# Kernel tuning notes

Measured on AMD Instinct MI355X. Metric: run time of the kernel, lower is better.

## Reference

```python
import jax, jax.numpy as jnp
import numpy as np
import math

D_MODEL = 256
N_HEADS = 8
HEAD_DIM = D_MODEL // N_HEADS  # 32
N_LEVELS = 4
N_POINTS = 4
SHAPES = [(112, 112), (56, 56), (28, 28), (14, 14)]
LEN_IN = sum(h * w for h, w in SHAPES)  # 16660
BATCH = 1
LEN_Q = LEN_IN


def _grid_init_bias():
    # Faithful to MSDeformAttn._reset_parameters: directional grid init for sampling_offsets bias.
    thetas = np.arange(N_HEADS, dtype=np.float32) * (2.0 * math.pi / N_HEADS)
    grid = np.stack([np.cos(thetas), np.sin(thetas)], -1)
    grid = grid / np.abs(grid).max(-1, keepdims=True)
    grid = np.tile(grid[:, None, None, :], (1, N_LEVELS, N_POINTS, 1)).copy()
    for i in range(N_POINTS):
        grid[:, :, i, :] *= i + 1
    return jnp.asarray(grid.reshape(-1), dtype=jnp.float32)


def setup_inputs() -> dict:
    key = jax.random.key(0)
    ks = jax.random.split(key, 10)
    s = 1.0 / math.sqrt(D_MODEL)
    return {
        "query": jax.random.normal(ks[0], (BATCH, LEN_Q, D_MODEL), jnp.float32),
        "reference_points": jax.random.uniform(ks[1], (BATCH, LEN_Q, N_LEVELS, 2), jnp.float32),
        "input_flatten": jax.random.normal(ks[2], (BATCH, LEN_IN, D_MODEL), jnp.float32),
        "spatial_shapes": jnp.asarray(SHAPES, dtype=jnp.int32),
        "level_start_index": jnp.asarray(np.cumsum([0] + [h * w for h, w in SHAPES])[:-1], dtype=jnp.int32),
        "W_q": jax.random.normal(ks[3], (D_MODEL, D_MODEL), jnp.float32) * s,
        "b_q": jnp.zeros((D_MODEL,), jnp.float32),
        "W_k": jax.random.normal(ks[4], (D_MODEL, D_MODEL), jnp.float32) * s,
        "b_k": jnp.zeros((D_MODEL,), jnp.float32),
        "W_v": jax.random.normal(ks[5], (D_MODEL, D_MODEL), jnp.float32) * s,
        "b_v": jnp.zeros((D_MODEL,), jnp.float32),
        "W_o": jax.random.normal(ks[6], (D_MODEL, D_MODEL), jnp.float32) * s,
        "b_o": jnp.zeros((D_MODEL,), jnp.float32),
        "W_off": jax.random.normal(ks[7], (D_MODEL, N_HEADS * N_LEVELS * N_POINTS * 2), jnp.float32) * 0.01,
        "b_off": _grid_init_bias(),
    }


def _bilinear_sample(img, grid, H, W):
    # img: (B, H*W, D) flattened feature map; grid: (B, Q, P, 2) in [-1, 1] (x, y order).
    # Matches F.grid_sample(mode='bilinear', padding_mode='zeros', align_corners=False).
    B, Q, P, _ = grid.shape
    x = ((grid[..., 0] + 1.0) * W - 1.0) * 0.5
    y = ((grid[..., 1] + 1.0) * H - 1.0) * 0.5
    x0 = jnp.floor(x)
    y0 = jnp.floor(y)
    lx = x - x0
    ly = y - y0
    x0i = x0.astype(jnp.int32)
    y0i = y0.astype(jnp.int32)

    def gather(yi, xi, w):
        valid = (xi >= 0) & (xi < W) & (yi >= 0) & (yi < H)
        idx = jnp.clip(yi, 0, H - 1) * W + jnp.clip(xi, 0, W - 1)
        v = jnp.take_along_axis(img, idx.reshape(B, Q * P, 1), axis=1)
        return v.reshape(B, Q, P, -1) * (w * valid)[..., None]

    return (gather(y0i, x0i, (1.0 - ly) * (1.0 - lx))
            + gather(y0i, x0i + 1, (1.0 - ly) * lx)
            + gather(y0i + 1, x0i, ly * (1.0 - lx))
            + gather(y0i + 1, x0i + 1, ly * lx))


def reference(query, reference_points, input_flatten, spatial_shapes, level_start_index,
              W_q, b_q, W_k, b_k, W_v, b_v, W_o, b_o, W_off, b_off):
    N, Lq, C = query.shape
    M, D, L, P = N_HEADS, HEAD_DIM, N_LEVELS, N_POINTS

    q = query @ W_q + b_q                                   # (N, Lq, C)
    value = (input_flatten @ W_v + b_v).reshape(N, -1, M, D)
    key_h = (input_flatten @ W_k + b_k).reshape(N, -1, M, D)

    offsets = (q @ W_off + b_off).reshape(N, Lq, M, L, P, 2)
    # offset_normalizer = (W_l, H_l) per level
    norm = jnp.stack([spatial_shapes[:, 1], spatial_shapes[:, 0]], -1).astype(q.dtype)
    loc = reference_points[:, :, None, :, None, :] + offsets / norm[None, None, None, :, None, :]
    grids = 2.0 * loc - 1.0                                  # (N, Lq, M, L, P, 2)

    samp_v, samp_k = [], []
    start = 0
    for lid, (H, W) in enumerate(SHAPES):
        end = start + H * W
        v_l = value[:, start:end].transpose(0, 2, 1, 3).reshape(N * M, H * W, D)
        k_l = key_h[:, start:end].transpose(0, 2, 1, 3).reshape(N * M, H * W, D)
        g_l = grids[:, :, :, lid].transpose(0, 2, 1, 3, 4).reshape(N * M, Lq, P, 2)
        samp_v.append(_bilinear_sample(v_l, g_l, H, W))      # (N*M, Lq, P, D)
        samp_k.append(_bilinear_sample(k_l, g_l, H, W))
        start = end

    v_s = jnp.stack(samp_v, axis=2).reshape(N, M, Lq, L, P, D)
    k_s = jnp.stack(samp_k, axis=2).reshape(N, M, Lq, L, P, D)

    qh = q.reshape(N, Lq, M, D)
    logits = jnp.einsum('nqmd,nmqlpd->nmqlp', qh, k_s) / math.sqrt(D)
    attn = jax.nn.softmax(logits.reshape(N, M, Lq, L * P), axis=-1).reshape(N, M, Lq, L, P)

    out = jnp.einsum('nmqlp,nmqlpd->nqmd', attn, v_s).reshape(N, Lq, C)
    return out @ W_o + b_o
```

## Files before the change

kernel.cpp:

```cpp
#include <hip/hip_runtime.h>
#include <hip/hip_bf16.h>
#include <math.h>

#define LEN_IN   16660
#define D_MODEL  256
#define N_HEADS  8
#define HEAD_DIM 32
#define N_LEVELS 4
#define N_POINTS 4

typedef __attribute__((ext_vector_type(8))) short short8v;
typedef __attribute__((ext_vector_type(4))) float f32x4;
typedef _Float16 f16x2 __attribute__((ext_vector_type(2)));
typedef _Float16 f16x8 __attribute__((ext_vector_type(8)));

__device__ __forceinline__ unsigned f2h16(float f) {
  _Float16 h = (_Float16)f;
  union { unsigned short u; _Float16 h; } c;
  c.h = h;
  return (unsigned)c.u;
}
__device__ __forceinline__ f16x2 u2h(unsigned u) {
  union { unsigned u; f16x2 h; } c;
  c.u = u;
  return c.h;
}

__global__ __launch_bounds__(256) void prep_B(
    const float* __restrict__ Wq, const float* __restrict__ Wk,
    const float* __restrict__ Wv, const float* __restrict__ Woff,
    const float* __restrict__ Wo,
    unsigned short* __restrict__ Btq, unsigned short* __restrict__ Btk,
    unsigned short* __restrict__ Btv, unsigned short* __restrict__ Btoff,
    unsigned short* __restrict__ Bto) {
  __shared__ float tile[64][65];
  int b = blockIdx.x;
  int mat = b >> 4, t = b & 15;
  int ti = t >> 2, tj = t & 3;
  const float* W = (mat == 0) ? Wq : (mat == 1) ? Wk : (mat == 2) ? Wv
                 : (mat == 3) ? Woff : Wo;
  unsigned short* Bt = (mat == 0) ? Btq : (mat == 1) ? Btk : (mat == 2) ? Btv
                     : (mat == 3) ? Btoff : Bto;
  int tid = threadIdx.x;
  #pragma unroll
  for (int i = 0; i < 16; i++) {
    int idx = tid + i * 256;
    int kr = idx >> 6, nc = idx & 63;
    tile[kr][nc] = W[(size_t)(ti * 64 + kr) * 256 + tj * 64 + nc];
  }
  __syncthreads();
  #pragma unroll
  for (int i = 0; i < 16; i++) {
    int idx = tid + i * 256;
    int nr = idx >> 6, kc = idx & 63;
    Bt[(size_t)(tj * 64 + nr) * 256 + ti * 64 + kc] =
        (unsigned short)f2h16(tile[kc][nr]);
  }
}

__global__ __launch_bounds__(256) void gemm_f16(
    const float* __restrict__ A,
    const unsigned short* __restrict__ Bt,
    const float* __restrict__ bias, float* __restrict__ C, int M) {
  const int P = 40;
  __shared__ short As[64 * P], Bs[64 * P];
  int tid = threadIdx.x;
  int m0 = blockIdx.x * 64, n0 = blockIdx.y * 64;
  int w = tid >> 6, l = tid & 63;
  int r = l & 15, g = l >> 4;
  int mi = (w >> 1) * 32, ni = (w & 1) * 32;
  int sm = tid >> 2, sp = tid & 3;

  f32x4 acc[2][2];
  #pragma unroll
  for (int a = 0; a < 2; a++)
    #pragma unroll
    for (int b = 0; b < 2; b++) acc[a][b] = (f32x4){0.f, 0.f, 0.f, 0.f};

  for (int k0 = 0; k0 < 256; k0 += 32) {
    int gm = m0 + sm;
    float f[8];
    if (gm < M) {
      const float* src = A + (size_t)gm * 256 + k0 + sp * 8;
      float4 u0 = *(const float4*)src;
      float4 u1 = *(const float4*)(src + 4);
      f[0] = u0.x; f[1] = u0.y; f[2] = u0.z; f[3] = u0.w;
      f[4] = u1.x; f[5] = u1.y; f[6] = u1.z; f[7] = u1.w;
    } else {
      #pragma unroll
      for (int j = 0; j < 8; j++) f[j] = 0.f;
    }
    f16x8 hv;
    #pragma unroll
    for (int j = 0; j < 8; j++) hv[j] = (_Float16)f[j];
    *(f16x8*)&As[sm * P + sp * 8] = hv;
    *(short8v*)&Bs[sm * P + sp * 8] =
        *(const short8v*)&Bt[(size_t)(n0 + sm) * 256 + k0 + sp * 8];
    __syncthreads();

    f16x8 af[2], bf[2];
    #pragma unroll
    for (int a = 0; a < 2; a++)
      af[a] = *(f16x8*)&As[(mi + a * 16 + r) * P + g * 8];
    #pragma unroll
    for (int b = 0; b < 2; b++)
      bf[b] = *(f16x8*)&Bs[(ni + b * 16 + r) * P + g * 8];
    #pragma unroll
    for (int a = 0; a < 2; a++)
      #pragma unroll
      for (int b = 0; b < 2; b++)
        acc[a][b] = __builtin_amdgcn_mfma_f32_16x16x32_f16(af[a], bf[b], acc[a][b], 0, 0, 0);
    __syncthreads();
  }

  #pragma unroll
  for (int a = 0; a < 2; a++)
    #pragma unroll
    for (int b = 0; b < 2; b++) {
      int col = n0 + ni + b * 16 + r;
      float bc = bias[col];
      #pragma unroll
      for (int i = 0; i < 4; i++) {
        int row = m0 + mi + a * 16 + g * 4 + i;
        if (row < M) C[(size_t)row * 256 + col] = acc[a][b][i] + bc;
      }
    }
}

__global__ __launch_bounds__(256) void gemm_kv_f16(
    const float* __restrict__ A,
    const unsigned short* __restrict__ Btk,
    const unsigned short* __restrict__ Btv,
    const float* __restrict__ bk, const float* __restrict__ bv,
    unsigned* __restrict__ kvout, int M) {
  const int P = 40;
  __shared__ short As[64 * P], Bks[64 * P], Bvs[64 * P];
  int tid = threadIdx.x;
  int m0 = blockIdx.x * 64, n0 = blockIdx.y * 64;
  int w = tid >> 6, l = tid & 63;
  int r = l & 15, g = l >> 4;
  int mi = (w >> 1) * 32, ni = (w & 1) * 32;
  int sm = tid >> 2, sp = tid & 3;

  f32x4 acck[2][2], accv[2][2];
  #pragma unroll
  for (int a = 0; a < 2; a++)
    #pragma unroll
    for (int b = 0; b < 2; b++) {
      acck[a][b] = (f32x4){0.f, 0.f, 0.f, 0.f};
      accv[a][b] = (f32x4){0.f, 0.f, 0.f, 0.f};
    }

  for (int k0 = 0; k0 < 256; k0 += 32) {
    int gm = m0 + sm;
    float f[8];
    if (gm < M) {
      const float* src = A + (size_t)gm * 256 + k0 + sp * 8;
      float4 u0 = *(const float4*)src;
      float4 u1 = *(const float4*)(src + 4);
      f[0] = u0.x; f[1] = u0.y; f[2] = u0.z; f[3] = u0.w;
      f[4] = u1.x; f[5] = u1.y; f[6] = u1.z; f[7] = u1.w;
    } else {
      #pragma unroll
      for (int j = 0; j < 8; j++) f[j] = 0.f;
    }
    f16x8 hv;
    #pragma unroll
    for (int j = 0; j < 8; j++) hv[j] = (_Float16)f[j];
    *(f16x8*)&As[sm * P + sp * 8] = hv;
    *(short8v*)&Bks[sm * P + sp * 8] =
        *(const short8v*)&Btk[(size_t)(n0 + sm) * 256 + k0 + sp * 8];
    *(short8v*)&Bvs[sm * P + sp * 8] =
        *(const short8v*)&Btv[(size_t)(n0 + sm) * 256 + k0 + sp * 8];
    __syncthreads();

    f16x8 af[2], fbk[2], fbv[2];
    #pragma unroll
    for (int a = 0; a < 2; a++)
      af[a] = *(f16x8*)&As[(mi + a * 16 + r) * P + g * 8];
    #pragma unroll
    for (int b = 0; b < 2; b++) {
      fbk[b] = *(f16x8*)&Bks[(ni + b * 16 + r) * P + g * 8];
      fbv[b] = *(f16x8*)&Bvs[(ni + b * 16 + r) * P + g * 8];
    }
    #pragma unroll
    for (int a = 0; a < 2; a++)
      #pragma unroll
      for (int b = 0; b < 2; b++) {
        acck[a][b] = __builtin_amdgcn_mfma_f32_16x16x32_f16(af[a], fbk[b], acck[a][b], 0, 0, 0);
        accv[a][b] = __builtin_amdgcn_mfma_f32_16x16x32_f16(af[a], fbv[b], accv[a][b], 0, 0, 0);
      }
    __syncthreads();
  }

  #pragma unroll
  for (int a = 0; a < 2; a++)
    #pragma unroll
    for (int b = 0; b < 2; b++) {
      int col = n0 + ni + b * 16 + r;
      float bkc = bk[col], bvc = bv[col];
      #pragma unroll
      for (int i = 0; i < 4; i++) {
        int row = m0 + mi + a * 16 + g * 4 + i;
        if (row < M) {
          unsigned kh = f2h16(acck[a][b][i] + bkc);
          unsigned vh = f2h16(accv[a][b][i] + bvc);
          kvout[(size_t)row * 256 + col] = kh | (vh << 16);
        }
      }
    }
}

__global__ __launch_bounds__(256) void sample_attn(
    const float* __restrict__ qp,
    const float* __restrict__ offs,
    const float* __restrict__ rp,
    const unsigned* __restrict__ kv,
    float* __restrict__ attn_out) {
  __shared__ float lbuf[4][16];
  __shared__ float ebuf[4][16];
  __shared__ float vbuf[4][16][36];

  int tid = threadIdx.x;
  int wslot = tid >> 6;
  int lane = tid & 63;
  int wid = blockIdx.x * 4 + wslot;
  int q = wid >> 3;
  int h = wid & 7;

  int pt = lane >> 2;
  int c8 = (lane & 3) * 8;
  int l5 = lane & 31;

  float offv = offs[(size_t)q * D_MODEL + h * 32 + l5];
  float rpv = (l5 < 8) ? rp[(size_t)q * 8 + l5] : 0.f;

  int l = pt >> 2, pp = pt & 3;
  int W = 112 >> l;
  int start = (int)((50176u - (50176u >> (2 * l))) / 3u);

  float off_x = __shfl(offv, l * 8 + pp * 2 + 0, 64);
  float off_y = __shfl(offv, l * 8 + pp * 2 + 1, 64);
  float rp_x = __shfl(rpv, l * 2 + 0, 64);
  float rp_y = __shfl(rpv, l * 2 + 1, 64);

  float x = rp_x * (float)W + off_x - 0.5f;
  float y = rp_y * (float)W + off_y - 0.5f;
  float x0f = floorf(x), y0f = floorf(y);
  float lx = x - x0f, ly = y - y0f;
  int x0 = (int)x0f, y0 = (int)y0f;
  float wx0 = 1.f - lx, wy0 = 1.f - ly;
  float tw[4] = {wy0 * wx0, wy0 * lx, ly * wx0, ly * lx};

  int hoff = h * 32 + c8;

  f16x2 acc[8];
  #pragma unroll
  for (int j = 0; j < 8; j++) acc[j] = (f16x2){(_Float16)0.f, (_Float16)0.f};

  #pragma unroll
  for (int tap = 0; tap < 4; tap++) {
    int yy = y0 + (tap >> 1), xx = x0 + (tap & 1);
    bool valid = ((unsigned)xx < (unsigned)W) & ((unsigned)yy < (unsigned)W);
    float wgt = valid ? tw[tap] : 0.f;
    int pix = valid ? (start + yy * W + xx) : start;
    const unsigned* p = kv + (size_t)pix * D_MODEL + hoff;
    uint4 u0 = *(const uint4*)p;
    uint4 u1 = *(const uint4*)(p + 4);
    _Float16 wh = (_Float16)wgt;
    f16x2 w2 = {wh, wh};
    acc[0] += w2 * u2h(u0.x);
    acc[1] += w2 * u2h(u0.y);
    acc[2] += w2 * u2h(u0.z);
    acc[3] += w2 * u2h(u0.w);
    acc[4] += w2 * u2h(u1.x);
    acc[5] += w2 * u2h(u1.y);
    acc[6] += w2 * u2h(u1.z);
    acc[7] += w2 * u2h(u1.w);
  }

  const float* qsrc = qp + (size_t)q * D_MODEL + hoff;
  float4 qa = *(const float4*)qsrc;
  float4 qb = *(const float4*)(qsrc + 4);
  float dot = qa.x * (float)acc[0][0] + qa.y * (float)acc[1][0]
            + qa.z * (float)acc[2][0] + qa.w * (float)acc[3][0]
            + qb.x * (float)acc[4][0] + qb.y * (float)acc[5][0]
            + qb.z * (float)acc[6][0] + qb.w * (float)acc[7][0];
  dot += __shfl_xor(dot, 1, 64);
  dot += __shfl_xor(dot, 2, 64);
  if ((lane & 3) == 0) lbuf[wslot][pt] = dot * 0.17677669529663687f;

  float4 v0 = {(float)acc[0][1], (float)acc[1][1], (float)acc[2][1], (float)acc[3][1]};
  float4 v1 = {(float)acc[4][1], (float)acc[5][1], (float)acc[6][1], (float)acc[7][1]};
  *(float4*)&vbuf[wslot][pt][c8] = v0;
  *(float4*)&vbuf[wslot][pt][c8 + 4] = v1;
  __syncthreads();

  float lg = lbuf[wslot][lane & 15];
  float m = lg;
  m = fmaxf(m, __shfl_xor(m, 1, 64));
  m = fmaxf(m, __shfl_xor(m, 2, 64));
  m = fmaxf(m, __shfl_xor(m, 4, 64));
  m = fmaxf(m, __shfl_xor(m, 8, 64));
  float e = __expf(lg - m);
  float s = e;
  s += __shfl_xor(s, 1, 64);
  s += __shfl_xor(s, 2, 64);
  s += __shfl_xor(s, 4, 64);
  s += __shfl_xor(s, 8, 64);
  if (lane < 16) ebuf[wslot][lane] = e;
  float inv = 1.f / s;
  __syncthreads();

  if (lane < 32) {
    float o = 0.f;
    #pragma unroll
    for (int p = 0; p < 16; p++) o += ebuf[wslot][p] * vbuf[wslot][p][lane];
    attn_out[(size_t)q * D_MODEL + h * 32 + lane] = o * inv;
  }
}

extern "C" void kernel_launch(void* const* d_in, const int* in_sizes, int n_in,
                              void* d_out, int out_size, void* d_ws, size_t ws_size,
                              hipStream_t stream) {
  const float* query = (const float*)d_in[0];
  const float* rp    = (const float*)d_in[1];
  const float* inp   = (const float*)d_in[2];
  const float* W_q   = (const float*)d_in[5];
  const float* b_q   = (const float*)d_in[6];
  const float* W_k   = (const float*)d_in[7];
  const float* b_k   = (const float*)d_in[8];
  const float* W_v   = (const float*)d_in[9];
  const float* b_v   = (const float*)d_in[10];
  const float* W_o   = (const float*)d_in[11];
  const float* b_o   = (const float*)d_in[12];
  const float* W_off = (const float*)d_in[13];
  const float* b_off = (const float*)d_in[14];
  float* out = (float*)d_out;

  const size_t nelem = (size_t)LEN_IN * D_MODEL;
  float* qp   = (float*)d_ws;
  float* offs = qp + nelem;
  float* attn = offs + nelem;
  unsigned* kvp = (unsigned*)(attn + nelem);
  unsigned short* Btq   = (unsigned short*)(kvp + nelem);
  unsigned short* Btk   = Btq + 256 * 256;
  unsigned short* Btv   = Btk + 256 * 256;
  unsigned short* Btoff = Btv + 256 * 256;
  unsigned short* Bto   = Btoff + 256 * 256;

  dim3 blk(256);
  dim3 ggrid((LEN_IN + 63) / 64, D_MODEL / 64);

  prep_B<<<80, blk, 0, stream>>>(W_q, W_k, W_v, W_off, W_o,
                                 Btq, Btk, Btv, Btoff, Bto);
  gemm_f16<<<ggrid, blk, 0, stream>>>(query, Btq, b_q, qp, LEN_IN);
  gemm_kv_f16<<<ggrid, blk, 0, stream>>>(inp, Btk, Btv, b_k, b_v, kvp, LEN_IN);
  gemm_f16<<<ggrid, blk, 0, stream>>>(qp, Btoff, b_off, offs, LEN_IN);

  int n_blocks = LEN_IN * N_HEADS / 4;
  sample_attn<<<n_blocks, blk, 0, stream>>>(qp, offs, rp, kvp, attn);

  gemm_f16<<<ggrid, blk, 0, stream>>>(attn, Bto, b_o, out, LEN_IN);
}
```

Before: 130.1 us.

## Store intermediates in fp16, split K/V planes, merge Q and KV GEMMs

```diff
diff --git a/kernel.cpp b/kernel.cpp
--- a/kernel.cpp
+++ b/kernel.cpp
@@ -6,19 +6,21 @@
 #define D_MODEL  256
 #define N_HEADS  8
 #define HEAD_DIM 32
-#define N_LEVELS 4
-#define N_POINTS 4
 
 typedef __attribute__((ext_vector_type(8))) short short8v;
 typedef __attribute__((ext_vector_type(4))) float f32x4;
 typedef _Float16 f16x2 __attribute__((ext_vector_type(2)));
 typedef _Float16 f16x8 __attribute__((ext_vector_type(8)));
 
-__device__ __forceinline__ unsigned f2h16(float f) {
-  _Float16 h = (_Float16)f;
+__device__ __forceinline__ unsigned short f2h(float f) {
   union { unsigned short u; _Float16 h; } c;
-  c.h = h;
-  return (unsigned)c.u;
+  c.h = (_Float16)f;
+  return c.u;
+}
+__device__ __forceinline__ float h2f(unsigned short u) {
+  union { unsigned short u; _Float16 h; } c;
+  c.u = u;
+  return (float)c.h;
 }
 __device__ __forceinline__ f16x2 u2h(unsigned u) {
   union { unsigned u; f16x2 h; } c;
@@ -53,17 +55,24 @@
   for (int i = 0; i < 16; i++) {
     int idx = tid + i * 256;
     int nr = idx >> 6, kc = idx & 63;
-    Bt[(size_t)(tj * 64 + nr) * 256 + ti * 64 + kc] =
-        (unsigned short)f2h16(tile[kc][nr]);
-  }
-}
-
-__global__ __launch_bounds__(256) void gemm_f16(
-    const float* __restrict__ A,
-    const unsigned short* __restrict__ Bt,
-    const float* __restrict__ bias, float* __restrict__ C, int M) {
+    Bt[(size_t)(tj * 64 + nr) * 256 + ti * 64 + kc] = f2h(tile[kc][nr]);
+  }
+}
+
+__global__ __launch_bounds__(256) void gemm_qkv(
+    const float* __restrict__ query, const float* __restrict__ inp,
+    const unsigned short* __restrict__ Btq,
+    const unsigned short* __restrict__ Btk,
+    const unsigned short* __restrict__ Btv,
+    const float* __restrict__ bq, const float* __restrict__ bk,
+    const float* __restrict__ bv,
+    unsigned short* __restrict__ qp_out,
+    unsigned short* __restrict__ k_out, unsigned short* __restrict__ v_out,
+    int M) {
   const int P = 40;
-  __shared__ short As[64 * P], Bs[64 * P];
+  __shared__ short As[64 * P], B1[64 * P], B2[64 * P];
+  bool isq = (blockIdx.z == 0);
+  const float* A = isq ? query : inp;
   int tid = threadIdx.x;
   int m0 = blockIdx.x * 64, n0 = blockIdx.y * 64;
   int w = tid >> 6, l = tid & 63;
@@ -71,11 +80,14 @@
   int mi = (w >> 1) * 32, ni = (w & 1) * 32;
   int sm = tid >> 2, sp = tid & 3;
 
-  f32x4 acc[2][2];
+  f32x4 acc1[2][2], acc2[2][2];
   #pragma unroll
   for (int a = 0; a < 2; a++)
     #pragma unroll
-    for (int b = 0; b < 2; b++) acc[a][b] = (f32x4){0.f, 0.f, 0.f, 0.f};
+    for (int b = 0; b < 2; b++) {
+      acc1[a][b] = (f32x4){0.f, 0.f, 0.f, 0.f};
+      acc2[a][b] = (f32x4){0.f, 0.f, 0.f, 0.f};
+    }
 
   for (int k0 = 0; k0 < 256; k0 += 32) {
     int gm = m0 + sm;
@@ -94,6 +106,92 @@
     #pragma unroll
     for (int j = 0; j < 8; j++) hv[j] = (_Float16)f[j];
     *(f16x8*)&As[sm * P + sp * 8] = hv;
+    if (isq) {
+      *(short8v*)&B1[sm * P + sp * 8] =
+          *(const short8v*)&Btq[(size_t)(n0 + sm) * 256 + k0 + sp * 8];
+    } else {
+      *(short8v*)&B1[sm * P + sp * 8] =
+          *(const short8v*)&Btk[(size_t)(n0 + sm) * 256 + k0 + sp * 8];
+      *(short8v*)&B2[sm * P + sp * 8] =
+          *(const short8v*)&Btv[(size_t)(n0 + sm) * 256 + k0 + sp * 8];
+    }
+    __syncthreads();
+
+    f16x8 af[2], b1f[2], b2f[2];
+    #pragma unroll
+    for (int a = 0; a < 2; a++)
+      af[a] = *(f16x8*)&As[(mi + a * 16 + r) * P + g * 8];
+    #pragma unroll
+    for (int b = 0; b < 2; b++)
+      b1f[b] = *(f16x8*)&B1[(ni + b * 16 + r) * P + g * 8];
+    if (!isq) {
+      #pragma unroll
+      for (int b = 0; b < 2; b++)
+        b2f[b] = *(f16x8*)&B2[(ni + b * 16 + r) * P + g * 8];
+    }
+    #pragma unroll
+    for (int a = 0; a < 2; a++)
+      #pragma unroll
+      for (int b = 0; b < 2; b++) {
+        acc1[a][b] = __builtin_amdgcn_mfma_f32_16x16x32_f16(af[a], b1f[b], acc1[a][b], 0, 0, 0);
+        if (!isq)
+          acc2[a][b] = __builtin_amdgcn_mfma_f32_16x16x32_f16(af[a], b2f[b], acc2[a][b], 0, 0, 0);
+      }
+    __syncthreads();
+  }
+
+  #pragma unroll
+  for (int a = 0; a < 2; a++)
+    #pragma unroll
+    for (int b = 0; b < 2; b++) {
+      int col = n0 + ni + b * 16 + r;
+      if (isq) {
+        float bc = bq[col];
+        #pragma unroll
+        for (int i = 0; i < 4; i++) {
+          int row = m0 + mi + a * 16 + g * 4 + i;
+          if (row < M) qp_out[(size_t)row * 256 + col] = f2h(acc1[a][b][i] + bc);
+        }
+      } else {
+        float bkc = bk[col], bvc = bv[col];
+        #pragma unroll
+        for (int i = 0; i < 4; i++) {
+          int row = m0 + mi + a * 16 + g * 4 + i;
+          if (row < M) {
+            k_out[(size_t)row * 256 + col] = f2h(acc1[a][b][i] + bkc);
+            v_out[(size_t)row * 256 + col] = f2h(acc2[a][b][i] + bvc);
+          }
+        }
+      }
+    }
+}
+
+template <bool OUT_F16>
+__global__ __launch_bounds__(256) void gemm_a16(
+    const unsigned short* __restrict__ A,
+    const unsigned short* __restrict__ Bt,
+    const float* __restrict__ bias, void* __restrict__ Cout, int M) {
+  const int P = 40;
+  __shared__ short As[64 * P], Bs[64 * P];
+  int tid = threadIdx.x;
+  int m0 = blockIdx.x * 64, n0 = blockIdx.y * 64;
+  int w = tid >> 6, l = tid & 63;
+  int r = l & 15, g = l >> 4;
+  int mi = (w >> 1) * 32, ni = (w & 1) * 32;
+  int sm = tid >> 2, sp = tid & 3;
+
+  f32x4 acc[2][2];
+  #pragma unroll
+  for (int a = 0; a < 2; a++)
+    #pragma unroll
+    for (int b = 0; b < 2; b++) acc[a][b] = (f32x4){0.f, 0.f, 0.f, 0.f};
+
+  for (int k0 = 0; k0 < 256; k0 += 32) {
+    int gm = m0 + sm;
+    short8v av = {0, 0, 0, 0, 0, 0, 0, 0};
+    if (gm < M)
+      av = *(const short8v*)&A[(size_t)gm * 256 + k0 + sp * 8];
+    *(short8v*)&As[sm * P + sp * 8] = av;
     *(short8v*)&Bs[sm * P + sp * 8] =
         *(const short8v*)&Bt[(size_t)(n0 + sm) * 256 + k0 + sp * 8];
     __syncthreads();
@@ -122,127 +220,50 @@
       #pragma unroll
       for (int i = 0; i < 4; i++) {
         int row = m0 + mi + a * 16 + g * 4 + i;
-        if (row < M) C[(size_t)row * 256 + col] = acc[a][b][i] + bc;
-      }
-    }
-}
-
-__global__ __launch_bounds__(256) void gemm_kv_f16(
-    const float* __restrict__ A,
-    const unsigned short* __restrict__ Btk,
-    const unsigned short* __restrict__ Btv,
-    const float* __restrict__ bk, const float* __restrict__ bv,
-    unsigned* __restrict__ kvout, int M) {
-  const int P = 40;
-  __shared__ short As[64 * P], Bks[64 * P], Bvs[64 * P];
-  int tid = threadIdx.x;
-  int m0 = blockIdx.x * 64, n0 = blockIdx.y * 64;
-  int w = tid >> 6, l = tid & 63;
-  int r = l & 15, g = l >> 4;
-  int mi = (w >> 1) * 32, ni = (w & 1) * 32;
-  int sm = tid >> 2, sp = tid & 3;
-
-  f32x4 acck[2][2], accv[2][2];
-  #pragma unroll
-  for (int a = 0; a < 2; a++)
-    #pragma unroll
-    for (int b = 0; b < 2; b++) {
-      acck[a][b] = (f32x4){0.f, 0.f, 0.f, 0.f};
-      accv[a][b] = (f32x4){0.f, 0.f, 0.f, 0.f};
-    }
-
-  for (int k0 = 0; k0 < 256; k0 += 32) {
-    int gm = m0 + sm;
-    float f[8];
-    if (gm < M) {
-      const float* src = A + (size_t)gm * 256 + k0 + sp * 8;
-      float4 u0 = *(const float4*)src;
-      float4 u1 = *(const float4*)(src + 4);
-      f[0] = u0.x; f[1] = u0.y; f[2] = u0.z; f[3] = u0.w;
-      f[4] = u1.x; f[5] = u1.y; f[6] = u1.z; f[7] = u1.w;
-    } else {
-      #pragma unroll
-      for (int j = 0; j < 8; j++) f[j] = 0.f;
-    }
-    f16x8 hv;
-    #pragma unroll
-    for (int j = 0; j < 8; j++) hv[j] = (_Float16)f[j];
-    *(f16x8*)&As[sm * P + sp * 8] = hv;
-    *(short8v*)&Bks[sm * P + sp * 8] =
-        *(const short8v*)&Btk[(size_t)(n0 + sm) * 256 + k0 + sp * 8];
-    *(short8v*)&Bvs[sm * P + sp * 8] =
-        *(const short8v*)&Btv[(size_t)(n0 + sm) * 256 + k0 + sp * 8];
-    __syncthreads();
-
-    f16x8 af[2], fbk[2], fbv[2];
-    #pragma unroll
-    for (int a = 0; a < 2; a++)
-      af[a] = *(f16x8*)&As[(mi + a * 16 + r) * P + g * 8];
-    #pragma unroll
-    for (int b = 0; b < 2; b++) {
-      fbk[b] = *(f16x8*)&Bks[(ni + b * 16 + r) * P + g * 8];
-      fbv[b] = *(f16x8*)&Bvs[(ni + b * 16 + r) * P + g * 8];
-    }
-    #pragma unroll
-    for (int a = 0; a < 2; a++)
-      #pragma unroll
-      for (int b = 0; b < 2; b++) {
-        acck[a][b] = __builtin_amdgcn_mfma_f32_16x16x32_f16(af[a], fbk[b], acck[a][b], 0, 0, 0);
-        accv[a][b] = __builtin_amdgcn_mfma_f32_16x16x32_f16(af[a], fbv[b], accv[a][b], 0, 0, 0);
-      }
-    __syncthreads();
-  }
-
-  #pragma unroll
-  for (int a = 0; a < 2; a++)
-    #pragma unroll
-    for (int b = 0; b < 2; b++) {
-      int col = n0 + ni + b * 16 + r;
-      float bkc = bk[col], bvc = bv[col];
-      #pragma unroll
-      for (int i = 0; i < 4; i++) {
-        int row = m0 + mi + a * 16 + g * 4 + i;
         if (row < M) {
-          unsigned kh = f2h16(acck[a][b][i] + bkc);
-          unsigned vh = f2h16(accv[a][b][i] + bvc);
-          kvout[(size_t)row * 256 + col] = kh | (vh << 16);
+          float v = acc[a][b][i] + bc;
+          if (OUT_F16)
+            ((unsigned short*)Cout)[(size_t)row * 256 + col] = f2h(v);
+          else
+            ((float*)Cout)[(size_t)row * 256 + col] = v;
         }
       }
     }
 }
 
 __global__ __launch_bounds__(256) void sample_attn(
-    const float* __restrict__ qp,
-    const float* __restrict__ offs,
+    const unsigned short* __restrict__ qp,
+    const unsigned short* __restrict__ offs,
     const float* __restrict__ rp,
-    const unsigned* __restrict__ kv,
-    float* __restrict__ attn_out) {
-  __shared__ float lbuf[4][16];
-  __shared__ float ebuf[4][16];
-  __shared__ float vbuf[4][16][36];
+    const unsigned short* __restrict__ kplane,
+    const unsigned short* __restrict__ vplane,
+    unsigned short* __restrict__ attn_out) {
+  __shared__ float lbuf[4][2][16];
+  __shared__ float ebuf[4][2][16];
+  __shared__ float vbuf[4][2][16][34];
 
   int tid = threadIdx.x;
   int wslot = tid >> 6;
   int lane = tid & 63;
-  int wid = blockIdx.x * 4 + wslot;
-  int q = wid >> 3;
-  int h = wid & 7;
-
-  int pt = lane >> 2;
-  int c8 = (lane & 3) * 8;
+  int qin = lane >> 5;
   int l5 = lane & 31;
-
-  float offv = offs[(size_t)q * D_MODEL + h * 32 + l5];
+  int pt = l5 >> 1;
+  int cp = lane & 1;
+  int widp = blockIdx.x * 8 + wslot * 2 + qin;
+  int q = widp >> 3;
+  int h = widp & 7;
+
+  float offv = h2f(offs[(size_t)q * 256 + h * 32 + l5]);
   float rpv = (l5 < 8) ? rp[(size_t)q * 8 + l5] : 0.f;
 
   int l = pt >> 2, pp = pt & 3;
   int W = 112 >> l;
   int start = (int)((50176u - (50176u >> (2 * l))) / 3u);
 
-  float off_x = __shfl(offv, l * 8 + pp * 2 + 0, 64);
-  float off_y = __shfl(offv, l * 8 + pp * 2 + 1, 64);
-  float rp_x = __shfl(rpv, l * 2 + 0, 64);
-  float rp_y = __shfl(rpv, l * 2 + 1, 64);
+  float off_x = __shfl(offv, l * 8 + pp * 2 + 0, 32);
+  float off_y = __shfl(offv, l * 8 + pp * 2 + 1, 32);
+  float rp_x = __shfl(rpv, l * 2 + 0, 32);
+  float rp_y = __shfl(rpv, l * 2 + 1, 32);
 
   float x = rp_x * (float)W + off_x - 0.5f;
   float y = rp_y * (float)W + off_y - 0.5f;
@@ -252,11 +273,14 @@
   float wx0 = 1.f - lx, wy0 = 1.f - ly;
   float tw[4] = {wy0 * wx0, wy0 * lx, ly * wx0, ly * lx};
 
-  int hoff = h * 32 + c8;
-
-  f16x2 acc[8];
-  #pragma unroll
-  for (int j = 0; j < 8; j++) acc[j] = (f16x2){(_Float16)0.f, (_Float16)0.f};
+  int coff = h * 32 + cp * 16;
+
+  f16x2 kacc[8], vacc[8];
+  #pragma unroll
+  for (int j = 0; j < 8; j++) {
+    kacc[j] = (f16x2){(_Float16)0.f, (_Float16)0.f};
+    vacc[j] = (f16x2){(_Float16)0.f, (_Float16)0.f};
+  }
 
   #pragma unroll
   for (int tap = 0; tap < 4; tap++) {
@@ -264,60 +288,70 @@
     bool valid = ((unsigned)xx < (unsigned)W) & ((unsigned)yy < (unsigned)W);
     float wgt = valid ? tw[tap] : 0.f;
     int pix = valid ? (start + yy * W + xx) : start;
-    const unsigned* p = kv + (size_t)pix * D_MODEL + hoff;
-    uint4 u0 = *(const uint4*)p;
-    uint4 u1 = *(const uint4*)(p + 4);
+    size_t base = (size_t)pix * 256 + coff;
+    uint4 k0 = *(const uint4*)(kplane + base);
+    uint4 k1 = *(const uint4*)(kplane + base + 8);
+    uint4 v0 = *(const uint4*)(vplane + base);
+    uint4 v1 = *(const uint4*)(vplane + base + 8);
     _Float16 wh = (_Float16)wgt;
     f16x2 w2 = {wh, wh};
-    acc[0] += w2 * u2h(u0.x);
-    acc[1] += w2 * u2h(u0.y);
-    acc[2] += w2 * u2h(u0.z);
-    acc[3] += w2 * u2h(u0.w);
-    acc[4] += w2 * u2h(u1.x);
-    acc[5] += w2 * u2h(u1.y);
-    acc[6] += w2 * u2h(u1.z);
-    acc[7] += w2 * u2h(u1.w);
-  }
-
-  const float* qsrc = qp + (size_t)q * D_MODEL + hoff;
-  float4 qa = *(const float4*)qsrc;
-  float4 qb = *(const float4*)(qsrc + 4);
-  float dot = qa.x * (float)acc[0][0] + qa.y * (float)acc[1][0]
-            + qa.z * (float)acc[2][0] + qa.w * (float)acc[3][0]
-            + qb.x * (float)acc[4][0] + qb.y * (float)acc[5][0]
-            + qb.z * (float)acc[6][0] + qb.w * (float)acc[7][0];
-  dot += __shfl_xor(dot, 1, 64);
-  dot += __shfl_xor(dot, 2, 64);
-  if ((lane & 3) == 0) lbuf[wslot][pt] = dot * 0.17677669529663687f;
-
-  float4 v0 = {(float)acc[0][1], (float)acc[1][1], (float)acc[2][1], (float)acc[3][1]};
-  float4 v1 = {(float)acc[4][1], (float)acc[5][1], (float)acc[6][1], (float)acc[7][1]};
-  *(float4*)&vbuf[wslot][pt][c8] = v0;
-  *(float4*)&vbuf[wslot][pt][c8 + 4] = v1;
+    kacc[0] += w2 * u2h(k0.x); kacc[1] += w2 * u2h(k0.y);
+    kacc[2] += w2 * u2h(k0.z); kacc[3] += w2 * u2h(k0.w);
+    kacc[4] += w2 * u2h(k1.x); kacc[5] += w2 * u2h(k1.y);
+    kacc[6] += w2 * u2h(k1.z); kacc[7] += w2 * u2h(k1.w);
+    vacc[0] += w2 * u2h(v0.x); vacc[1] += w2 * u2h(v0.y);
+    vacc[2] += w2 * u2h(v0.z); vacc[3] += w2 * u2h(v0.w);
+    vacc[4] += w2 * u2h(v1.x); vacc[5] += w2 * u2h(v1.y);
+    vacc[6] += w2 * u2h(v1.z); vacc[7] += w2 * u2h(v1.w);
+  }
+
+  const uint4* qsrc = (const uint4*)(qp + (size_t)q * 256 + coff);
+  uint4 qa = qsrc[0], qb = qsrc[1];
+  float dot = 0.f;
+  dot = __builtin_amdgcn_fdot2(u2h(qa.x), kacc[0], dot, false);
+  dot = __builtin_amdgcn_fdot2(u2h(qa.y), kacc[1], dot, false);
+  dot = __builtin_amdgcn_fdot2(u2h(qa.z), kacc[2], dot, false);
+  dot = __builtin_amdgcn_fdot2(u2h(qa.w), kacc[3], dot, false);
+  dot = __builtin_amdgcn_fdot2(u2h(qb.x), kacc[4], dot, false);
+  dot = __builtin_amdgcn_fdot2(u2h(qb.y), kacc[5], dot, false);
+  dot = __builtin_amdgcn_fdot2(u2h(qb.z), kacc[6], dot, false);
+  dot = __builtin_amdgcn_fdot2(u2h(qb.w), kacc[7], dot, false);
+  dot += __shfl_xor(dot, 1, 32);
+  if (cp == 0) lbuf[wslot][qin][pt] = dot * 0.17677669529663687f;
+
+  float4 w0 = {(float)vacc[0][0], (float)vacc[0][1], (float)vacc[1][0], (float)vacc[1][1]};
+  float4 w1 = {(float)vacc[2][0], (float)vacc[2][1], (float)vacc[3][0], (float)vacc[3][1]};
+  float4 w2_ = {(float)vacc[4][0], (float)vacc[4][1], (float)vacc[5][0], (float)vacc[5][1]};
+  float4 w3 = {(float)vacc[6][0], (float)vacc[6][1], (float)vacc[7][0], (float)vacc[7][1]};
+  float* vdst = &vbuf[wslot][qin][pt][cp * 16];
+  *(float4*)(vdst + 0) = w0;
+  *(float4*)(vdst + 4) = w1;
+  *(float4*)(vdst + 8) = w2_;
+  *(float4*)(vdst + 12) = w3;
   __syncthreads();
 
-  float lg = lbuf[wslot][lane & 15];
+  float lg = lbuf[wslot][qin][lane & 15];
   float m = lg;
-  m = fmaxf(m, __shfl_xor(m, 1, 64));
-  m = fmaxf(m, __shfl_xor(m, 2, 64));
-  m = fmaxf(m, __shfl_xor(m, 4, 64));
-  m = fmaxf(m, __shfl_xor(m, 8, 64));
+  m = fmaxf(m, __shfl_xor(m, 1, 32));
+  m = fmaxf(m, __shfl_xor(m, 2, 32));
+  m = fmaxf(m, __shfl_xor(m, 4, 32));
+  m = fmaxf(m, __shfl_xor(m, 8, 32));
   float e = __expf(lg - m);
   float s = e;
-  s += __shfl_xor(s, 1, 64);
-  s += __shfl_xor(s, 2, 64);
-  s += __shfl_xor(s, 4, 64);
-  s += __shfl_xor(s, 8, 64);
-  if (lane < 16) ebuf[wslot][lane] = e;
+  s += __shfl_xor(s, 1, 32);
+  s += __shfl_xor(s, 2, 32);
+  s += __shfl_xor(s, 4, 32);
+  s += __shfl_xor(s, 8, 32);
+  if ((lane & 16) == 0) ebuf[wslot][qin][lane & 15] = e;
   float inv = 1.f / s;
   __syncthreads();
 
-  if (lane < 32) {
-    float o = 0.f;
-    #pragma unroll
-    for (int p = 0; p < 16; p++) o += ebuf[wslot][p] * vbuf[wslot][p][lane];
-    attn_out[(size_t)q * D_MODEL + h * 32 + lane] = o * inv;
-  }
+  int c = lane & 31;
+  float o = 0.f;
+  #pragma unroll
+  for (int p = 0; p < 16; p++)
+    o += ebuf[wslot][qin][p] * vbuf[wslot][qin][p][c];
+  attn_out[(size_t)q * 256 + h * 32 + c] = f2h(o * inv);
 }
 
 extern "C" void kernel_launch(void* const* d_in, const int* in_sizes, int n_in,
@@ -339,11 +373,12 @@
   float* out = (float*)d_out;
 
   const size_t nelem = (size_t)LEN_IN * D_MODEL;
-  float* qp   = (float*)d_ws;
-  float* offs = qp + nelem;
-  float* attn = offs + nelem;
-  unsigned* kvp = (unsigned*)(attn + nelem);
-  unsigned short* Btq   = (unsigned short*)(kvp + nelem);
+  unsigned short* qp    = (unsigned short*)d_ws;
+  unsigned short* offsb = qp + nelem;
+  unsigned short* attn  = offsb + nelem;
+  unsigned short* kpl   = attn + nelem;
+  unsigned short* vpl   = kpl + nelem;
+  unsigned short* Btq   = vpl + nelem;
   unsigned short* Btk   = Btq + 256 * 256;
   unsigned short* Btv   = Btk + 256 * 256;
   unsigned short* Btoff = Btv + 256 * 256;
@@ -351,15 +386,15 @@
 
   dim3 blk(256);
   dim3 ggrid((LEN_IN + 63) / 64, D_MODEL / 64);
+  dim3 ggrid2((LEN_IN + 63) / 64, D_MODEL / 64, 2);
 
   prep_B<<<80, blk, 0, stream>>>(W_q, W_k, W_v, W_off, W_o,
                                  Btq, Btk, Btv, Btoff, Bto);
-  gemm_f16<<<ggrid, blk, 0, stream>>>(query, Btq, b_q, qp, LEN_IN);
-  gemm_kv_f16<<<ggrid, blk, 0, stream>>>(inp, Btk, Btv, b_k, b_v, kvp, LEN_IN);
-  gemm_f16<<<ggrid, blk, 0, stream>>>(qp, Btoff, b_off, offs, LEN_IN);
-
-  int n_blocks = LEN_IN * N_HEADS / 4;
-  sample_attn<<<n_blocks, blk, 0, stream>>>(qp, offs, rp, kvp, attn);
-
-  gemm_f16<<<ggrid, blk, 0, stream>>>(attn, Bto, b_o, out, LEN_IN);
-}
+  gemm_qkv<<<ggrid2, blk, 0, stream>>>(query, inp, Btq, Btk, Btv,
+                                       b_q, b_k, b_v, qp, kpl, vpl, LEN_IN);
+  gemm_a16<true><<<ggrid, blk, 0, stream>>>(qp, Btoff, b_off, offsb, LEN_IN);
+
+  sample_attn<<<LEN_IN, blk, 0, stream>>>(qp, offsb, rp, kpl, vpl, attn);
+
+  gemm_a16<false><<<ggrid, blk, 0, stream>>>(attn, Bto, b_o, out, LEN_IN);
+}
```

Result: slower. 163.1 us (+25.3%).
